# Optimization experiments

Hardware: AMD Instinct MI355X
Metric: run time of the kernel (lower is better)

The kernel has to match this reference:

```python
import jax, jax.numpy as jnp
import numpy as np

N = 50000   # nodes
E = 800000  # edges (before self-loops)
IN, H1, H2, OUT = 128, 256, 256, 64


def _gcn_layer(x, src, dst, norm_src, norm_dst, W, b, act):
    # DGL GraphConv, norm='both': D_in^{-1/2} * A^T * (D_out^{-1/2} * x) @ W + b
    x = x * norm_src                                   # [N, d_in]
    m = jax.ops.segment_sum(x[src], dst, num_segments=N)  # gather + scatter-add
    h = (m * norm_dst) @ W + b                         # [N, d_out]
    return act(h) if act is not None else h


def setup_inputs() -> dict:
    key = jax.random.key(0)
    ks = jax.random.split(key, 9)
    feats = jax.random.normal(ks[0], (N, IN), dtype=jnp.float32)
    src = jax.random.randint(ks[1], (E,), 0, N, dtype=jnp.int32)
    dst = jax.random.randint(ks[2], (E,), 0, N, dtype=jnp.int32)
    # avoid pre-existing self-loops (forward removes then re-adds exactly one per node)
    dst = jnp.where(src == dst, (dst + 1) % N, dst)
    def glorot(k, fi, fo):
        lim = float(np.sqrt(6.0 / (fi + fo)))
        return jax.random.uniform(k, (fi, fo), jnp.float32, -lim, lim)
    return {
        "feats": feats,
        "W1": glorot(ks[3], IN, H1), "b1": jnp.zeros((H1,), jnp.float32),
        "W2": glorot(ks[4], H1, H2), "b2": jnp.zeros((H2,), jnp.float32),
        "W3": glorot(ks[5], H2, OUT), "b3": jnp.zeros((OUT,), jnp.float32),
        "src": src, "dst": dst,
    }


def reference(feats, W1, b1, W2, b2, W3, b3, src, dst):
    # add self-loops
    loops = jnp.arange(N, dtype=src.dtype)
    s = jnp.concatenate([src, loops])
    d = jnp.concatenate([dst, loops])
    ones = jnp.ones(s.shape[0], jnp.float32)
    out_deg = jax.ops.segment_sum(ones, s, num_segments=N)
    in_deg = jax.ops.segment_sum(ones, d, num_segments=N)
    norm_src = (out_deg ** -0.5)[:, None]
    norm_dst = (in_deg ** -0.5)[:, None]
    relu = jax.nn.relu
    h = _gcn_layer(feats, s, d, norm_src, norm_dst, W1, b1, relu)
    # dropout p=0.0 (eval) is identity
    h = _gcn_layer(h, s, d, norm_src, norm_dst, W2, b2, relu)
    h = _gcn_layer(h, s, d, norm_src, norm_dst, W3, b3, None)
    return h
```

## Files before the change

### kernel.cpp

```cpp
#include <hip/hip_runtime.h>
#include <hip/hip_fp16.h>
#include <stdint.h>

#define NODES 50000
#define F_IN 128
#define F_H1 256
#define F_H2 256
#define F_OUT 64
#define SLICES 64
#define NPACK (NODES / 2)
#define QPACK (NPACK / 4)

using f32x4    = __attribute__((ext_vector_type(4))) float;
using f16x8    = __attribute__((ext_vector_type(8))) _Float16;
using ushort8v = __attribute__((ext_vector_type(8))) unsigned short;

__global__ __launch_bounds__(512) void k_hist2(
    const int* __restrict__ src, const int* __restrict__ dst,
    unsigned* __restrict__ p_out, unsigned* __restrict__ p_in, int e) {
  __shared__ unsigned bo[QPACK];
  __shared__ unsigned bi[QPACK];
  const int s = blockIdx.x >> 2;
  const int r = blockIdx.x & 3;
  const int nlo = r * (NODES / 4);
  const int nhi = nlo + NODES / 4;
  const int plo = r * QPACK;
  const int per = (e + SLICES - 1) / SLICES;
  const int beg = s * per;
  const int end = min(e, beg + per);

  for (int j = threadIdx.x; j < QPACK; j += 512) { bo[j] = 0; bi[j] = 0; }
  __syncthreads();
  for (int i = beg + (int)threadIdx.x; i < end; i += 512) {
    int a = src[i];
    if (a >= nlo && a < nhi)
      atomicAdd(&bo[(a >> 1) - plo], 1u << ((a & 1) << 4));
    int d = dst[i];
    if (d >= nlo && d < nhi)
      atomicAdd(&bi[(d >> 1) - plo], 1u << ((d & 1) << 4));
  }
  __syncthreads();
  for (int j = threadIdx.x; j < QPACK; j += 512) {
    p_out[(size_t)s * NPACK + plo + j] = bo[j];
    p_in[(size_t)s * NPACK + plo + j] = bi[j];
  }
}

__global__ __launch_bounds__(256) void k_degnorm(
    const unsigned* __restrict__ p_out, const unsigned* __restrict__ p_in,
    unsigned* __restrict__ base_in, int* __restrict__ deg_in,
    float* __restrict__ ns, float* __restrict__ nd) {
  int p = blockIdx.x * 256 + threadIdx.x;
  if (p >= NPACK) return;
  unsigned so = 0, si = 0;
#pragma unroll 4
  for (int s = 0; s < SLICES; ++s) {
    so += p_out[(size_t)s * NPACK + p];
    unsigned vi = p_in[(size_t)s * NPACK + p];
    base_in[(size_t)s * NPACK + p] = si;
    si += vi;
  }
  int o0 = (int)(so & 0xFFFFu) + 1, o1 = (int)(so >> 16) + 1;
  int i0 = (int)(si & 0xFFFFu) + 1, i1 = (int)(si >> 16) + 1;
  int n0 = p * 2, n1 = n0 + 1;
  deg_in[n0] = i0; deg_in[n1] = i1;
  ns[n0] = rsqrtf((float)o0); ns[n1] = rsqrtf((float)o1);
  nd[n0] = rsqrtf((float)i0); nd[n1] = rsqrtf((float)i1);
}

__global__ __launch_bounds__(256) void k_scan1(const int* __restrict__ deg_in,
                                               int* __restrict__ psum, int n) {
  int i = blockIdx.x * 256 + threadIdx.x;
  int v = (i < n) ? deg_in[i] - 1 : 0;
#pragma unroll
  for (int o = 1; o < 64; o <<= 1) v += __shfl_xor(v, o);
  __shared__ int ws[4];
  if ((threadIdx.x & 63) == 0) ws[threadIdx.x >> 6] = v;
  __syncthreads();
  if (threadIdx.x == 0) psum[blockIdx.x] = ws[0] + ws[1] + ws[2] + ws[3];
}

__global__ __launch_bounds__(256) void k_scan2(int* __restrict__ psum, int nb) {
  __shared__ int s[256];
  int t = threadIdx.x;
  int v = (t < nb) ? psum[t] : 0;
  s[t] = v;
  __syncthreads();
  for (int o = 1; o < 256; o <<= 1) {
    int u = (t >= o) ? s[t - o] : 0;
    __syncthreads();
    s[t] += u;
    __syncthreads();
  }
  if (t < nb) psum[t] = s[t] - v;
}

__global__ __launch_bounds__(256) void k_scan3(const int* __restrict__ deg_in,
                                               const int* __restrict__ psum,
                                               int* __restrict__ row_ptr, int n) {
  int i = blockIdx.x * 256 + threadIdx.x;
  int lane = threadIdx.x & 63;
  int w = threadIdx.x >> 6;
  int v = (i < n) ? deg_in[i] - 1 : 0;
  int x = v;
#pragma unroll
  for (int o = 1; o < 64; o <<= 1) {
    int u = __shfl_up(x, o);
    if (lane >= o) x += u;
  }
  __shared__ int wsum[4];
  if (lane == 63) wsum[w] = x;
  __syncthreads();
  int woff = 0;
#pragma unroll
  for (int j = 0; j < 4; ++j)
    if (j < w) woff += wsum[j];
  int excl = x - v + woff + psum[blockIdx.x];
  if (i < n) row_ptr[i] = excl;
  if (i == n - 1) row_ptr[n] = excl + v;
}

__global__ __launch_bounds__(512) void k_scatter4(
    const int* __restrict__ src, const int* __restrict__ dst,
    const int* __restrict__ row_ptr, const unsigned* __restrict__ base_in,
    int* __restrict__ csr_src, int e) {
  __shared__ unsigned cur[QPACK];
  const int s = blockIdx.x >> 2;
  const int r = blockIdx.x & 3;
  const int nlo = r * (NODES / 4);
  const int nhi = nlo + NODES / 4;
  const int plo = r * QPACK;
  const int per = (e + SLICES - 1) / SLICES;
  const int beg = s * per;
  const int end = min(e, beg + per);
  for (int j = threadIdx.x; j < QPACK; j += 512)
    cur[j] = base_in[(size_t)s * NPACK + plo + j];
  __syncthreads();
  for (int i = beg + (int)threadIdx.x; i < end; i += 512) {
    int d = dst[i];
    if (d >= nlo && d < nhi) {
      int sh = (d & 1) << 4;
      unsigned old = atomicAdd(&cur[(d >> 1) - plo], 1u << sh);
      int local = (int)((old >> sh) & 0xFFFFu);
      csr_src[row_ptr[d] + local] = src[i];
    }
  }
}

__global__ void k_prescale_h(const float* __restrict__ X, const float* __restrict__ ns,
                             __half* __restrict__ Y, int total4) {
  int i = blockIdx.x * blockDim.x + threadIdx.x;
  if (i < total4) {
    int row = i >> 5;
    float s = ns[row];
    float4 v = reinterpret_cast<const float4*>(X)[i];
    __half2 h0 = __floats2half2_rn(v.x * s, v.y * s);
    __half2 h1 = __floats2half2_rn(v.z * s, v.w * s);
    union { struct { __half2 a, b; } h; uint2 u; } o;
    o.h.a = h0; o.h.b = h1;
    reinterpret_cast<uint2*>(Y)[i] = o.u;
  }
}

__global__ void k_wprep_h(const float* __restrict__ W, __half* __restrict__ Wt,
                          int K, int NOUT) {
  int i = blockIdx.x * blockDim.x + threadIdx.x;
  if (i < K * NOUT) {
    int k = i / NOUT, n = i % NOUT;
    Wt[(size_t)n * K + k] = __float2half_rn(W[i]);
  }
}

struct u32x8s { uint4 a, b; };
template <int HPL> struct raw_t_sel;
template <> struct raw_t_sel<2> { using type = unsigned int; };
template <> struct raw_t_sel<4> { using type = uint2; };
template <> struct raw_t_sel<8> { using type = uint4; };
template <> struct raw_t_sel<16> { using type = u32x8s; };

template <int HPL>
__device__ __forceinline__ typename raw_t_sel<HPL>::type graw(const __half* p) {
  if constexpr (HPL == 16) {
    u32x8s r;
    r.a = *reinterpret_cast<const uint4*>(p);
    r.b = *reinterpret_cast<const uint4*>(p + 8);
    return r;
  } else {
    return *reinterpret_cast<const typename raw_t_sel<HPL>::type*>(p);
  }
}
__device__ __forceinline__ void acc_u32(float* acc, unsigned u) {
  union { unsigned u; __half2 h; } a; a.u = u;
  float2 f = __half22float2(a.h);
  acc[0] += f.x; acc[1] += f.y;
}
template <int HPL>
__device__ __forceinline__ void raw_acc(float* acc, typename raw_t_sel<HPL>::type r) {
  if constexpr (HPL == 16) {
    acc_u32(acc + 0, r.a.x);  acc_u32(acc + 2, r.a.y);
    acc_u32(acc + 4, r.a.z);  acc_u32(acc + 6, r.a.w);
    acc_u32(acc + 8, r.b.x);  acc_u32(acc + 10, r.b.y);
    acc_u32(acc + 12, r.b.z); acc_u32(acc + 14, r.b.w);
  } else if constexpr (HPL == 8) {
    acc_u32(acc + 0, r.x); acc_u32(acc + 2, r.y);
    acc_u32(acc + 4, r.z); acc_u32(acc + 6, r.w);
  } else if constexpr (HPL == 4) {
    acc_u32(acc + 0, r.x); acc_u32(acc + 2, r.y);
  } else {
    acc_u32(acc, r);
  }
}

template <int D, int EPI, bool BIAS, bool OHALF>
__global__ __launch_bounds__(256) void k_spmm_h(
    const __half* __restrict__ X, const int* __restrict__ row_ptr,
    const int* __restrict__ csr_src, const float* __restrict__ nd,
    const float* __restrict__ bias, void* __restrict__ Y, int n) {
  constexpr int LPN = 64 / EPI;
  constexpr int HPL = D / LPN;
  static_assert(HPL >= 2 && HPL <= 16, "bad HPL");
  const int v = (blockIdx.x * blockDim.x + threadIdx.x) >> 6;
  const int lane = threadIdx.x & 63;
  if (v >= n) return;
  const int sub = lane / LPN;
  const int fl = lane % LPN;
  const int off = fl * HPL;
  const __half* __restrict__ Xo = X + off;

  float acc[HPL] = {};
  if (sub == 0) raw_acc<HPL>(acc, graw<HPL>(Xo + (size_t)v * D));

  const int beg = row_ptr[v];
  const int end = row_ptr[v + 1];
#pragma unroll 2
  for (int e = beg + sub; e < end; e += EPI) {
    int u = csr_src[e];
    raw_acc<HPL>(acc, graw<HPL>(Xo + (size_t)u * D));
  }

#pragma unroll
  for (int o = LPN; o < 64; o <<= 1)
#pragma unroll
    for (int i = 0; i < HPL; ++i) acc[i] += __shfl_xor(acc[i], o);

  if (sub != 0) return;
  const float sc = nd[v];
  float o[HPL];
#pragma unroll
  for (int i = 0; i < HPL; ++i) {
    o[i] = sc * acc[i];
    if (BIAS) o[i] += bias[off + i];
  }

  if constexpr (OHALF) {
    __half* yp = reinterpret_cast<__half*>(Y) + (size_t)v * D + off;
    if constexpr (HPL == 16) {
      union { struct { __half2 a, b, c, d; } h; uint4 u; } p0, p1;
      p0.h.a = __floats2half2_rn(o[0], o[1]);
      p0.h.b = __floats2half2_rn(o[2], o[3]);
      p0.h.c = __floats2half2_rn(o[4], o[5]);
      p0.h.d = __floats2half2_rn(o[6], o[7]);
      p1.h.a = __floats2half2_rn(o[8], o[9]);
      p1.h.b = __floats2half2_rn(o[10], o[11]);
      p1.h.c = __floats2half2_rn(o[12], o[13]);
      p1.h.d = __floats2half2_rn(o[14], o[15]);
      *reinterpret_cast<uint4*>(yp) = p0.u;
      *reinterpret_cast<uint4*>(yp + 8) = p1.u;
    } else if constexpr (HPL == 8) {
      union { struct { __half2 a, b, c, d; } h; uint4 u; } pk;
      pk.h.a = __floats2half2_rn(o[0], o[1]);
      pk.h.b = __floats2half2_rn(o[2], o[3]);
      pk.h.c = __floats2half2_rn(o[4], o[5]);
      pk.h.d = __floats2half2_rn(o[6], o[7]);
      *reinterpret_cast<uint4*>(yp) = pk.u;
    } else if constexpr (HPL == 4) {
      union { struct { __half2 a, b; } h; uint2 u; } pk;
      pk.h.a = __floats2half2_rn(o[0], o[1]);
      pk.h.b = __floats2half2_rn(o[2], o[3]);
      *reinterpret_cast<uint2*>(yp) = pk.u;
    } else {
      *reinterpret_cast<__half2*>(yp) = __floats2half2_rn(o[0], o[1]);
    }
  } else {
    float* yp = reinterpret_cast<float*>(Y) + (size_t)v * D + off;
    if constexpr (HPL == 8) {
      *reinterpret_cast<float4*>(yp) = make_float4(o[0], o[1], o[2], o[3]);
      *reinterpret_cast<float4*>(yp + 4) = make_float4(o[4], o[5], o[6], o[7]);
    } else if constexpr (HPL == 4) {
      *reinterpret_cast<float4*>(yp) = make_float4(o[0], o[1], o[2], o[3]);
    } else {
      *reinterpret_cast<float2*>(yp) = make_float2(o[0], o[1]);
    }
  }
}

template <int K, int NOUT, int BM, int WM, int WN, int MF, int NF,
          bool RELU, bool BIAS, bool NSOUT, bool OHALF>
__global__ __launch_bounds__(256) void k_gemm_h(
    const __half* __restrict__ A, const __half* __restrict__ Wt,
    const float* __restrict__ bias, const float* __restrict__ ns,
    void* __restrict__ C, int M) {
  constexpr int BN = WN * NF * 16;
  static_assert(BM == WM * MF * 16, "BM mismatch");
  static_assert(BN == NOUT, "BN must equal NOUT");
  constexpr int LDP = 40;

  __shared__ __half As[BM][LDP];
  __shared__ __half Ws[BN][LDP];

  const int tid = threadIdx.x;
  const int bm = blockIdx.x * BM;
  const int lane = tid & 63;
  const int wave = tid >> 6;
  const int wmi = wave / WN;
  const int wni = wave % WN;
  const int rl = lane & 15;
  const int kg = lane >> 4;
  const int kb = kg * 8;

  f32x4 acc[MF][NF];
#pragma unroll
  for (int m = 0; m < MF; ++m)
#pragma unroll
    for (int n = 0; n < NF; ++n) acc[m][n] = (f32x4){0.f, 0.f, 0.f, 0.f};

  for (int kk = 0; kk < K; kk += 32) {
#pragma unroll
    for (int s0 = 0; s0 < BM * 4; s0 += 256) {
      int s = s0 + tid;
      int r = s >> 2, c8 = (s & 3) << 3;
      int grow = bm + r;
      ushort8v v = (ushort8v){0, 0, 0, 0, 0, 0, 0, 0};
      if (grow < M)
        v = *reinterpret_cast<const ushort8v*>(A + (size_t)grow * K + kk + c8);
      *reinterpret_cast<ushort8v*>(&As[r][c8]) = v;
    }
#pragma unroll
    for (int s0 = 0; s0 < BN * 4; s0 += 256) {
      int s = s0 + tid;
      int nn = s >> 2, k8 = (s & 3) << 3;
      *reinterpret_cast<ushort8v*>(&Ws[nn][k8]) =
          *reinterpret_cast<const ushort8v*>(Wt + (size_t)nn * K + kk + k8);
    }
    __syncthreads();

    f16x8 af[MF], bf[NF];
#pragma unroll
    for (int m = 0; m < MF; ++m) {
      const int r = wmi * MF * 16 + m * 16 + rl;
      af[m] = *reinterpret_cast<const f16x8*>(&As[r][kb]);
    }
#pragma unroll
    for (int n = 0; n < NF; ++n) {
      const int c = wni * NF * 16 + n * 16 + rl;
      bf[n] = *reinterpret_cast<const f16x8*>(&Ws[c][kb]);
    }
#pragma unroll
    for (int m = 0; m < MF; ++m)
#pragma unroll
      for (int n = 0; n < NF; ++n)
        acc[m][n] = __builtin_amdgcn_mfma_f32_16x16x32_f16(af[m], bf[n], acc[m][n], 0, 0, 0);
    __syncthreads();
  }

#pragma unroll
  for (int m = 0; m < MF; ++m) {
#pragma unroll
    for (int n = 0; n < NF; ++n) {
      const int col = wni * NF * 16 + n * 16 + rl;
      const float bb = BIAS ? bias[col] : 0.f;
      const int rowbase = bm + wmi * MF * 16 + m * 16 + kg * 4;
#pragma unroll
      for (int i = 0; i < 4; ++i) {
        int grow = rowbase + i;
        if (grow < M) {
          float val = acc[m][n][i] + bb;
          if (RELU) val = fmaxf(val, 0.f);
          if (NSOUT) val *= ns[grow];
          if constexpr (OHALF)
            reinterpret_cast<__half*>(C)[(size_t)grow * NOUT + col] = __float2half_rn(val);
          else
            reinterpret_cast<float*>(C)[(size_t)grow * NOUT + col] = val;
        }
      }
    }
  }
}

extern "C" void kernel_launch(void* const* d_in, const int* in_sizes, int n_in,
                              void* d_out, int out_size, void* d_ws, size_t ws_size,
                              hipStream_t stream) {
  const float* feats = (const float*)d_in[0];
  const float* W1 = (const float*)d_in[1];
  const float* b1 = (const float*)d_in[2];
  const float* W2 = (const float*)d_in[3];
  const float* b2 = (const float*)d_in[4];
  const float* W3 = (const float*)d_in[5];
  const float* b3 = (const float*)d_in[6];
  const int* src = (const int*)d_in[7];
  const int* dst = (const int*)d_in[8];
  float* out = (float*)d_out;
  const int N = NODES;
  const int E = in_sizes[7];
  const int NB = (N + 255) / 256;

  char* ws = (char*)d_ws;
  size_t off = 0;
  auto alloc = [&](size_t bytes) -> void* {
    void* p = ws + off;
    off += (bytes + 255) & ~(size_t)255;
    return p;
  };
  __half* w0h = (__half*)alloc((size_t)N * 256 * sizeof(__half));
  __half* w1r = (__half*)alloc((size_t)N * 256 * sizeof(__half));
  __half* w2r = (__half*)alloc((size_t)N * 256 * sizeof(__half));
  int* deg_in = (int*)alloc((size_t)N * sizeof(int));
  float* ns = (float*)alloc((size_t)N * sizeof(float));
  float* nd = (float*)alloc((size_t)N * sizeof(float));
  int* row_ptr = (int*)alloc((size_t)(N + 1) * sizeof(int));
  int* csr_src = (int*)alloc((size_t)E * sizeof(int));
  int* psum = (int*)alloc((size_t)NB * sizeof(int));
  unsigned* p_out = (unsigned*)alloc((size_t)SLICES * NPACK * sizeof(unsigned));
  unsigned* p_in = (unsigned*)alloc((size_t)SLICES * NPACK * sizeof(unsigned));
  unsigned* base_in = (unsigned*)alloc((size_t)SLICES * NPACK * sizeof(unsigned));
  __half* wt1 = (__half*)alloc((size_t)F_IN * F_H1 * sizeof(__half));
  __half* wt2 = (__half*)alloc((size_t)F_H1 * F_H2 * sizeof(__half));
  __half* wt3 = (__half*)alloc((size_t)F_H2 * F_OUT * sizeof(__half));
  (void)ws_size; (void)n_in; (void)out_size;

  hipLaunchKernelGGL(k_wprep_h, dim3((F_IN * F_H1 + 255) / 256), dim3(256), 0, stream,
                     W1, wt1, F_IN, F_H1);
  hipLaunchKernelGGL(k_wprep_h, dim3((F_H1 * F_H2 + 255) / 256), dim3(256), 0, stream,
                     W2, wt2, F_H1, F_H2);
  hipLaunchKernelGGL(k_wprep_h, dim3((F_H2 * F_OUT + 255) / 256), dim3(256), 0, stream,
                     W3, wt3, F_H2, F_OUT);

  hipLaunchKernelGGL(k_hist2, dim3(SLICES * 4), dim3(512), 0, stream,
                     src, dst, p_out, p_in, E);
  hipLaunchKernelGGL(k_degnorm, dim3((NPACK + 255) / 256), dim3(256), 0, stream,
                     p_out, p_in, base_in, deg_in, ns, nd);
  hipLaunchKernelGGL(k_scan1, dim3(NB), dim3(256), 0, stream, deg_in, psum, N);
  hipLaunchKernelGGL(k_scan2, dim3(1), dim3(256), 0, stream, psum, NB);
  hipLaunchKernelGGL(k_scan3, dim3(NB), dim3(256), 0, stream, deg_in, psum, row_ptr, N);
  hipLaunchKernelGGL(k_scatter4, dim3(SLICES * 4), dim3(512), 0, stream,
                     src, dst, row_ptr, base_in, csr_src, E);

  hipLaunchKernelGGL(k_prescale_h, dim3((N * 32 + 255) / 256), dim3(256), 0, stream,
                     feats, ns, w2r, N * 32);

  auto grid_w = [](int waves) { return dim3((waves + 3) / 4); };

  hipLaunchKernelGGL((k_spmm_h<128, 8, false, true>), grid_w(N), dim3(256), 0, stream,
                     w2r, row_ptr, csr_src, nd, nullptr, w1r, N);
  hipLaunchKernelGGL((k_gemm_h<128, 256, 64, 1, 4, 4, 4, true, true, true, true>),
                     dim3((N + 63) / 64), dim3(256), 0, stream,
                     w1r, wt1, b1, ns, w2r, N);

  hipLaunchKernelGGL((k_spmm_h<256, 4, false, true>), grid_w(N), dim3(256), 0, stream,
                     w2r, row_ptr, csr_src, nd, nullptr, w0h, N);
  hipLaunchKernelGGL((k_gemm_h<256, 256, 64, 1, 4, 4, 4, true, true, true, true>),
                     dim3((N + 63) / 64), dim3(256), 0, stream,
                     w0h, wt2, b2, ns, w1r, N);

  hipLaunchKernelGGL((k_gemm_h<256, 64, 128, 4, 1, 2, 4, false, false, false, true>),
                     dim3((N + 127) / 128), dim3(256), 0, stream,
                     w1r, wt3, nullptr, nullptr, w2r, N);
  hipLaunchKernelGGL((k_spmm_h<64, 8, true, false>), grid_w(N), dim3(256), 0, stream,
                     w2r, row_ptr, csr_src, nd, b3, out, N);
}
```

Baseline: 261.8 us.

## Fuse SpMM aggregation with GEMM for layers one and two; merge weight prep

Adds a fused kernel that gathers and aggregates neighbour rows for a 64-node tile straight into shared memory, then runs an MFMA GEMM with bias, ReLU and source-norm scaling. This removes the intermediate aggregated-feature buffer round trip through global memory and one launch per layer. The three weight-transpose launches are also merged into one. In exchange, each wave now processes 16 nodes serially in the gather phase, and the GEMM stage reloads weight tiles with a sync every K step and writes scalar half outputs, which may reduce gather parallelism and store efficiency.

```diff
diff --git a/kernel.cpp b/kernel.cpp
--- a/kernel.cpp
+++ b/kernel.cpp
@@ -162,12 +162,21 @@
   }
 }
 
-__global__ void k_wprep_h(const float* __restrict__ W, __half* __restrict__ Wt,
-                          int K, int NOUT) {
-  int i = blockIdx.x * blockDim.x + threadIdx.x;
-  if (i < K * NOUT) {
-    int k = i / NOUT, n = i % NOUT;
-    Wt[(size_t)n * K + k] = __float2half_rn(W[i]);
+__global__ void k_wprep_all(const float* __restrict__ W1, const float* __restrict__ W2,
+                            const float* __restrict__ W3, __half* __restrict__ wt1,
+                            __half* __restrict__ wt2, __half* __restrict__ wt3) {
+  int i = blockIdx.x * 256 + threadIdx.x;
+  if (i < F_IN * F_H1) {
+    int k = i >> 8, n = i & 255;
+    wt1[(size_t)n * F_IN + k] = __float2half_rn(W1[i]);
+  } else if (i < F_IN * F_H1 + F_H1 * F_H2) {
+    int j = i - F_IN * F_H1;
+    int k = j >> 8, n = j & 255;
+    wt2[(size_t)n * F_H1 + k] = __float2half_rn(W2[j]);
+  } else if (i < F_IN * F_H1 + F_H1 * F_H2 + F_H2 * F_OUT) {
+    int j = i - F_IN * F_H1 - F_H1 * F_H2;
+    int k = j >> 6, n = j & 63;
+    wt3[(size_t)n * F_H2 + k] = __float2half_rn(W3[j]);
   }
 }
 
@@ -208,6 +217,118 @@
     acc_u32(acc + 0, r.x); acc_u32(acc + 2, r.y);
   } else {
     acc_u32(acc, r);
+  }
+}
+
+template <int K>
+__global__ __launch_bounds__(256) void k_fused(
+    const __half* __restrict__ X, const int* __restrict__ row_ptr,
+    const int* __restrict__ csr_src, const float* __restrict__ nd,
+    const __half* __restrict__ Wt, const float* __restrict__ bias,
+    const float* __restrict__ ns, __half* __restrict__ C, int M) {
+  constexpr int BN = 256;
+  constexpr int LPN = K / 16;
+  constexpr int EPI = 64 / LPN;
+  constexpr int LDPA = K + 8;
+  constexpr int LDPB = 40;
+
+  __shared__ __half As[64][LDPA];
+  __shared__ __half Ws[BN][LDPB];
+
+  const int tid = threadIdx.x;
+  const int bm = blockIdx.x * 64;
+  const int lane = tid & 63;
+  const int wave = tid >> 6;
+  const int sub = lane / LPN;
+  const int fl = lane % LPN;
+  const int off = fl * 16;
+
+  for (int t = 0; t < 16; ++t) {
+    const int r = wave * 16 + t;
+    const int v = bm + r;
+    float acc[16] = {};
+    if (v < M) {
+      const __half* __restrict__ Xo = X + off;
+      if (sub == 0) raw_acc<16>(acc, graw<16>(Xo + (size_t)v * K));
+      const int beg = row_ptr[v];
+      const int end = row_ptr[v + 1];
+#pragma unroll 2
+      for (int e = beg + sub; e < end; e += EPI)
+        raw_acc<16>(acc, graw<16>(Xo + (size_t)csr_src[e] * K));
+    }
+#pragma unroll
+    for (int o = LPN; o < 64; o <<= 1)
+#pragma unroll
+      for (int i = 0; i < 16; ++i) acc[i] += __shfl_xor(acc[i], o);
+    if (sub == 0) {
+      const float sc = (v < M) ? nd[v] : 0.f;
+      union { struct { __half2 a, b, c, d; } h; uint4 u; } p0, p1;
+      p0.h.a = __floats2half2_rn(sc * acc[0], sc * acc[1]);
+      p0.h.b = __floats2half2_rn(sc * acc[2], sc * acc[3]);
+      p0.h.c = __floats2half2_rn(sc * acc[4], sc * acc[5]);
+      p0.h.d = __floats2half2_rn(sc * acc[6], sc * acc[7]);
+      p1.h.a = __floats2half2_rn(sc * acc[8], sc * acc[9]);
+      p1.h.b = __floats2half2_rn(sc * acc[10], sc * acc[11]);
+      p1.h.c = __floats2half2_rn(sc * acc[12], sc * acc[13]);
+      p1.h.d = __floats2half2_rn(sc * acc[14], sc * acc[15]);
+      *reinterpret_cast<uint4*>(&As[r][off]) = p0.u;
+      *reinterpret_cast<uint4*>(&As[r][off + 8]) = p1.u;
+    }
+  }
+  __syncthreads();
+
+  const int wni = wave;
+  const int rl = lane & 15;
+  const int kg = lane >> 4;
+  const int kb = kg * 8;
+
+  f32x4 acc2[4][4];
+#pragma unroll
+  for (int m = 0; m < 4; ++m)
+#pragma unroll
+    for (int n = 0; n < 4; ++n) acc2[m][n] = (f32x4){0.f, 0.f, 0.f, 0.f};
+
+  for (int kk = 0; kk < K; kk += 32) {
+#pragma unroll
+    for (int s0 = 0; s0 < BN * 4; s0 += 256) {
+      int s = s0 + tid;
+      int nn = s >> 2, k8 = (s & 3) << 3;
+      *reinterpret_cast<ushort8v*>(&Ws[nn][k8]) =
+          *reinterpret_cast<const ushort8v*>(Wt + (size_t)nn * K + kk + k8);
+    }
+    __syncthreads();
+
+    f16x8 af[4], bf[4];
+#pragma unroll
+    for (int m = 0; m < 4; ++m)
+      af[m] = *reinterpret_cast<const f16x8*>(&As[m * 16 + rl][kk + kb]);
+#pragma unroll
+    for (int n = 0; n < 4; ++n)
+      bf[n] = *reinterpret_cast<const f16x8*>(&Ws[wni * 64 + n * 16 + rl][kb]);
+#pragma unroll
+    for (int m = 0; m < 4; ++m)
+#pragma unroll
+      for (int n = 0; n < 4; ++n)
+        acc2[m][n] = __builtin_amdgcn_mfma_f32_16x16x32_f16(af[m], bf[n], acc2[m][n], 0, 0, 0);
+    __syncthreads();
+  }
+
+#pragma unroll
+  for (int m = 0; m < 4; ++m) {
+#pragma unroll
+    for (int n = 0; n < 4; ++n) {
+      const int col = wni * 64 + n * 16 + rl;
+      const float bb = bias[col];
+      const int rowbase = bm + m * 16 + kg * 4;
+#pragma unroll
+      for (int i = 0; i < 4; ++i) {
+        int grow = rowbase + i;
+        if (grow < M) {
+          float val = fmaxf(acc2[m][n][i] + bb, 0.f) * ns[grow];
+          C[(size_t)grow * BN + col] = __float2half_rn(val);
+        }
+      }
+    }
   }
 }
 
@@ -254,19 +375,7 @@
 
   if constexpr (OHALF) {
     __half* yp = reinterpret_cast<__half*>(Y) + (size_t)v * D + off;
-    if constexpr (HPL == 16) {
-      union { struct { __half2 a, b, c, d; } h; uint4 u; } p0, p1;
-      p0.h.a = __floats2half2_rn(o[0], o[1]);
-      p0.h.b = __floats2half2_rn(o[2], o[3]);
-      p0.h.c = __floats2half2_rn(o[4], o[5]);
-      p0.h.d = __floats2half2_rn(o[6], o[7]);
-      p1.h.a = __floats2half2_rn(o[8], o[9]);
-      p1.h.b = __floats2half2_rn(o[10], o[11]);
-      p1.h.c = __floats2half2_rn(o[12], o[13]);
-      p1.h.d = __floats2half2_rn(o[14], o[15]);
-      *reinterpret_cast<uint4*>(yp) = p0.u;
-      *reinterpret_cast<uint4*>(yp + 8) = p1.u;
-    } else if constexpr (HPL == 8) {
+    if constexpr (HPL == 8) {
       union { struct { __half2 a, b, c, d; } h; uint4 u; } pk;
       pk.h.a = __floats2half2_rn(o[0], o[1]);
       pk.h.b = __floats2half2_rn(o[2], o[3]);
@@ -428,12 +537,9 @@
   __half* wt3 = (__half*)alloc((size_t)F_H2 * F_OUT * sizeof(__half));
   (void)ws_size; (void)n_in; (void)out_size;
 
-  hipLaunchKernelGGL(k_wprep_h, dim3((F_IN * F_H1 + 255) / 256), dim3(256), 0, stream,
-                     W1, wt1, F_IN, F_H1);
-  hipLaunchKernelGGL(k_wprep_h, dim3((F_H1 * F_H2 + 255) / 256), dim3(256), 0, stream,
-                     W2, wt2, F_H1, F_H2);
-  hipLaunchKernelGGL(k_wprep_h, dim3((F_H2 * F_OUT + 255) / 256), dim3(256), 0, stream,
-                     W3, wt3, F_H2, F_OUT);
+  const int WPTOT = F_IN * F_H1 + F_H1 * F_H2 + F_H2 * F_OUT;
+  hipLaunchKernelGGL(k_wprep_all, dim3((WPTOT + 255) / 256), dim3(256), 0, stream,
+                     W1, W2, W3, wt1, wt2, wt3);
 
   hipLaunchKernelGGL(k_hist2, dim3(SLICES * 4), dim3(512), 0, stream,
                      src, dst, p_out, p_in, E);
@@ -448,23 +554,15 @@
   hipLaunchKernelGGL(k_prescale_h, dim3((N * 32 + 255) / 256), dim3(256), 0, stream,
                      feats, ns, w2r, N * 32);
 
-  auto grid_w = [](int waves) { return dim3((waves + 3) / 4); };
-
-  hipLaunchKernelGGL((k_spmm_h<128, 8, false, true>), grid_w(N), dim3(256), 0, stream,
-                     w2r, row_ptr, csr_src, nd, nullptr, w1r, N);
-  hipLaunchKernelGGL((k_gemm_h<128, 256, 64, 1, 4, 4, 4, true, true, true, true>),
-                     dim3((N + 63) / 64), dim3(256), 0, stream,
-                     w1r, wt1, b1, ns, w2r, N);
-
-  hipLaunchKernelGGL((k_spmm_h<256, 4, false, true>), grid_w(N), dim3(256), 0, stream,
-                     w2r, row_ptr, csr_src, nd, nullptr, w0h, N);
-  hipLaunchKernelGGL((k_gemm_h<256, 256, 64, 1, 4, 4, 4, true, true, true, true>),
-                     dim3((N + 63) / 64), dim3(256), 0, stream,
-                     w0h, wt2, b2, ns, w1r, N);
+  hipLaunchKernelGGL((k_fused<128>), dim3((N + 63) / 64), dim3(256), 0, stream,
+                     w2r, row_ptr, csr_src, nd, wt1, b1, ns, w1r, N);
+
+  hipLaunchKernelGGL((k_fused<256>), dim3((N + 63) / 64), dim3(256), 0, stream,
+                     w1r, row_ptr, csr_src, nd, wt2, b2, ns, w0h, N);
 
   hipLaunchKernelGGL((k_gemm_h<256, 64, 128, 4, 1, 2, 4, false, false, false, true>),
                      dim3((N + 127) / 128), dim3(256), 0, stream,
-                     w1r, wt3, nullptr, nullptr, w2r, N);
-  hipLaunchKernelGGL((k_spmm_h<64, 8, true, false>), grid_w(N), dim3(256), 0, stream,
+                     w0h, wt3, nullptr, nullptr, w2r, N);
+  hipLaunchKernelGGL((k_spmm_h<64, 8, true, false>), dim3((N + 3) / 4), dim3(256), 0, stream,
                      w2r, row_ptr, csr_src, nd, b3, out, N);
 }
```

Measured after the change: 352.2 us. +34.5%, slower.

## Fuse degree-norm and scan into one cooperative kernel; merge weight prep into prescale

Applied to the files above, without the earlier changes.

Replaces the degnorm plus three-kernel scan chain with a single cooperative kernel that computes norms, does block-local scans, takes a grid sync, then turns block sums into row pointers. The three weight transpose/convert launches are folded into the feature prescale kernel. The aim is fewer kernel launches and less launch/serialization overhead in the preprocessing stage. The price is a grid-wide barrier and a cooperative launch that needs all 196 blocks co-resident.

```diff
diff --git a/kernel.cpp b/kernel.cpp
--- a/kernel.cpp
+++ b/kernel.cpp
@@ -1,6 +1,9 @@
 #include <hip/hip_runtime.h>
 #include <hip/hip_fp16.h>
+#include <hip/hip_cooperative_groups.h>
 #include <stdint.h>
+
+namespace cg = cooperative_groups;
 
 #define NODES 50000
 #define F_IN 128
@@ -10,6 +13,7 @@
 #define SLICES 64
 #define NPACK (NODES / 2)
 #define QPACK (NPACK / 4)
+#define META_B 196
 
 using f32x4    = __attribute__((ext_vector_type(4))) float;
 using f16x8    = __attribute__((ext_vector_type(8))) _Float16;
@@ -46,78 +50,70 @@
   }
 }
 
-__global__ __launch_bounds__(256) void k_degnorm(
+__global__ __launch_bounds__(256) void k_csrmeta(
     const unsigned* __restrict__ p_out, const unsigned* __restrict__ p_in,
-    unsigned* __restrict__ base_in, int* __restrict__ deg_in,
-    float* __restrict__ ns, float* __restrict__ nd) {
-  int p = blockIdx.x * 256 + threadIdx.x;
-  if (p >= NPACK) return;
-  unsigned so = 0, si = 0;
+    unsigned* __restrict__ base_in, float* __restrict__ ns, float* __restrict__ nd,
+    int* __restrict__ psum, int* __restrict__ row_ptr) {
+  const int b = blockIdx.x;
+  const int t = threadIdx.x;
+  const int lane = t & 63;
+  const int w = t >> 6;
+  __shared__ int degm1[256];
+  __shared__ int wsum[4];
+  __shared__ int bsum[4];
+
+  int d0 = 0, d1 = 0;
+  if (t < 128) {
+    int p = b * 128 + t;
+    if (p < NPACK) {
+      unsigned so = 0, si = 0;
 #pragma unroll 4
-  for (int s = 0; s < SLICES; ++s) {
-    so += p_out[(size_t)s * NPACK + p];
-    unsigned vi = p_in[(size_t)s * NPACK + p];
-    base_in[(size_t)s * NPACK + p] = si;
-    si += vi;
-  }
-  int o0 = (int)(so & 0xFFFFu) + 1, o1 = (int)(so >> 16) + 1;
-  int i0 = (int)(si & 0xFFFFu) + 1, i1 = (int)(si >> 16) + 1;
-  int n0 = p * 2, n1 = n0 + 1;
-  deg_in[n0] = i0; deg_in[n1] = i1;
-  ns[n0] = rsqrtf((float)o0); ns[n1] = rsqrtf((float)o1);
-  nd[n0] = rsqrtf((float)i0); nd[n1] = rsqrtf((float)i1);
-}
-
-__global__ __launch_bounds__(256) void k_scan1(const int* __restrict__ deg_in,
-                                               int* __restrict__ psum, int n) {
-  int i = blockIdx.x * 256 + threadIdx.x;
-  int v = (i < n) ? deg_in[i] - 1 : 0;
-#pragma unroll
-  for (int o = 1; o < 64; o <<= 1) v += __shfl_xor(v, o);
-  __shared__ int ws[4];
-  if ((threadIdx.x & 63) == 0) ws[threadIdx.x >> 6] = v;
-  __syncthreads();
-  if (threadIdx.x == 0) psum[blockIdx.x] = ws[0] + ws[1] + ws[2] + ws[3];
-}
-
-__global__ __launch_bounds__(256) void k_scan2(int* __restrict__ psum, int nb) {
-  __shared__ int s[256];
-  int t = threadIdx.x;
-  int v = (t < nb) ? psum[t] : 0;
-  s[t] = v;
-  __syncthreads();
-  for (int o = 1; o < 256; o <<= 1) {
-    int u = (t >= o) ? s[t - o] : 0;
-    __syncthreads();
-    s[t] += u;
-    __syncthreads();
-  }
-  if (t < nb) psum[t] = s[t] - v;
-}
-
-__global__ __launch_bounds__(256) void k_scan3(const int* __restrict__ deg_in,
-                                               const int* __restrict__ psum,
-                                               int* __restrict__ row_ptr, int n) {
-  int i = blockIdx.x * 256 + threadIdx.x;
-  int lane = threadIdx.x & 63;
-  int w = threadIdx.x >> 6;
-  int v = (i < n) ? deg_in[i] - 1 : 0;
+      for (int s = 0; s < SLICES; ++s) {
+        so += p_out[(size_t)s * NPACK + p];
+        unsigned vi = p_in[(size_t)s * NPACK + p];
+        base_in[(size_t)s * NPACK + p] = si;
+        si += vi;
+      }
+      int o0 = (int)(so & 0xFFFFu) + 1, o1 = (int)(so >> 16) + 1;
+      int i0 = (int)(si & 0xFFFFu) + 1, i1 = (int)(si >> 16) + 1;
+      int n0 = p * 2, n1 = n0 + 1;
+      ns[n0] = rsqrtf((float)o0); ns[n1] = rsqrtf((float)o1);
+      nd[n0] = rsqrtf((float)i0); nd[n1] = rsqrtf((float)i1);
+      d0 = i0 - 1; d1 = i1 - 1;
+    }
+    degm1[2 * t] = d0;
+    degm1[2 * t + 1] = d1;
+  }
+  __syncthreads();
+
+  const int v = degm1[t];
   int x = v;
 #pragma unroll
   for (int o = 1; o < 64; o <<= 1) {
     int u = __shfl_up(x, o);
     if (lane >= o) x += u;
   }
-  __shared__ int wsum[4];
   if (lane == 63) wsum[w] = x;
   __syncthreads();
+  if (t == 0) psum[b] = wsum[0] + wsum[1] + wsum[2] + wsum[3];
+
+  cg::this_grid().sync();
+
+  int pv = (t < b) ? psum[t] : 0;
+#pragma unroll
+  for (int o = 1; o < 64; o <<= 1) pv += __shfl_xor(pv, o);
+  if (lane == 0) bsum[w] = pv;
+  __syncthreads();
+  const int prefix = bsum[0] + bsum[1] + bsum[2] + bsum[3];
+
   int woff = 0;
 #pragma unroll
   for (int j = 0; j < 4; ++j)
     if (j < w) woff += wsum[j];
-  int excl = x - v + woff + psum[blockIdx.x];
-  if (i < n) row_ptr[i] = excl;
-  if (i == n - 1) row_ptr[n] = excl + v;
+  const int excl = (x - v) + woff + prefix;
+  const int node = b * 256 + t;
+  if (node < NODES) row_ptr[node] = excl;
+  if (node == NODES - 1) row_ptr[NODES] = excl + v;
 }
 
 __global__ __launch_bounds__(512) void k_scatter4(
@@ -147,10 +143,14 @@
   }
 }
 
-__global__ void k_prescale_h(const float* __restrict__ X, const float* __restrict__ ns,
-                             __half* __restrict__ Y, int total4) {
-  int i = blockIdx.x * blockDim.x + threadIdx.x;
-  if (i < total4) {
+#define WPTOT (F_IN * F_H1 + F_H1 * F_H2 + F_H2 * F_OUT)
+__global__ void k_prewprep(const float* __restrict__ X, const float* __restrict__ ns,
+                           __half* __restrict__ Y,
+                           const float* __restrict__ W1, const float* __restrict__ W2,
+                           const float* __restrict__ W3, __half* __restrict__ wt1,
+                           __half* __restrict__ wt2, __half* __restrict__ wt3) {
+  int i = blockIdx.x * 256 + threadIdx.x;
+  if (i < NODES * 32) {
     int row = i >> 5;
     float s = ns[row];
     float4 v = reinterpret_cast<const float4*>(X)[i];
@@ -160,14 +160,19 @@
     o.h.a = h0; o.h.b = h1;
     reinterpret_cast<uint2*>(Y)[i] = o.u;
   }
-}
-
-__global__ void k_wprep_h(const float* __restrict__ W, __half* __restrict__ Wt,
-                          int K, int NOUT) {
-  int i = blockIdx.x * blockDim.x + threadIdx.x;
-  if (i < K * NOUT) {
-    int k = i / NOUT, n = i % NOUT;
-    Wt[(size_t)n * K + k] = __float2half_rn(W[i]);
+  if (i < WPTOT) {
+    if (i < F_IN * F_H1) {
+      int k = i >> 8, n = i & 255;
+      wt1[(size_t)n * F_IN + k] = __float2half_rn(W1[i]);
+    } else if (i < F_IN * F_H1 + F_H1 * F_H2) {
+      int j = i - F_IN * F_H1;
+      int k = j >> 8, n = j & 255;
+      wt2[(size_t)n * F_H1 + k] = __float2half_rn(W2[j]);
+    } else {
+      int j = i - F_IN * F_H1 - F_H1 * F_H2;
+      int k = j >> 6, n = j & 63;
+      wt3[(size_t)n * F_H2 + k] = __float2half_rn(W3[j]);
+    }
   }
 }
 
@@ -402,7 +407,6 @@
   float* out = (float*)d_out;
   const int N = NODES;
   const int E = in_sizes[7];
-  const int NB = (N + 255) / 256;
 
   char* ws = (char*)d_ws;
   size_t off = 0;
@@ -414,12 +418,11 @@
   __half* w0h = (__half*)alloc((size_t)N * 256 * sizeof(__half));
   __half* w1r = (__half*)alloc((size_t)N * 256 * sizeof(__half));
   __half* w2r = (__half*)alloc((size_t)N * 256 * sizeof(__half));
-  int* deg_in = (int*)alloc((size_t)N * sizeof(int));
   float* ns = (float*)alloc((size_t)N * sizeof(float));
   float* nd = (float*)alloc((size_t)N * sizeof(float));
   int* row_ptr = (int*)alloc((size_t)(N + 1) * sizeof(int));
   int* csr_src = (int*)alloc((size_t)E * sizeof(int));
-  int* psum = (int*)alloc((size_t)NB * sizeof(int));
+  int* psum = (int*)alloc((size_t)META_B * sizeof(int));
   unsigned* p_out = (unsigned*)alloc((size_t)SLICES * NPACK * sizeof(unsigned));
   unsigned* p_in = (unsigned*)alloc((size_t)SLICES * NPACK * sizeof(unsigned));
   unsigned* base_in = (unsigned*)alloc((size_t)SLICES * NPACK * sizeof(unsigned));
@@ -428,25 +431,20 @@
   __half* wt3 = (__half*)alloc((size_t)F_H2 * F_OUT * sizeof(__half));
   (void)ws_size; (void)n_in; (void)out_size;
 
-  hipLaunchKernelGGL(k_wprep_h, dim3((F_IN * F_H1 + 255) / 256), dim3(256), 0, stream,
-                     W1, wt1, F_IN, F_H1);
-  hipLaunchKernelGGL(k_wprep_h, dim3((F_H1 * F_H2 + 255) / 256), dim3(256), 0, stream,
-                     W2, wt2, F_H1, F_H2);
-  hipLaunchKernelGGL(k_wprep_h, dim3((F_H2 * F_OUT + 255) / 256), dim3(256), 0, stream,
-                     W3, wt3, F_H2, F_OUT);
-
   hipLaunchKernelGGL(k_hist2, dim3(SLICES * 4), dim3(512), 0, stream,
                      src, dst, p_out, p_in, E);
-  hipLaunchKernelGGL(k_degnorm, dim3((NPACK + 255) / 256), dim3(256), 0, stream,
-                     p_out, p_in, base_in, deg_in, ns, nd);
-  hipLaunchKernelGGL(k_scan1, dim3(NB), dim3(256), 0, stream, deg_in, psum, N);
-  hipLaunchKernelGGL(k_scan2, dim3(1), dim3(256), 0, stream, psum, NB);
-  hipLaunchKernelGGL(k_scan3, dim3(NB), dim3(256), 0, stream, deg_in, psum, row_ptr, N);
+
+  {
+    void* args[] = {(void*)&p_out, (void*)&p_in, (void*)&base_in, (void*)&ns,
+                    (void*)&nd, (void*)&psum, (void*)&row_ptr};
+    hipLaunchCooperativeKernel((void*)k_csrmeta, dim3(META_B), dim3(256), args, 0, stream);
+  }
+
   hipLaunchKernelGGL(k_scatter4, dim3(SLICES * 4), dim3(512), 0, stream,
                      src, dst, row_ptr, base_in, csr_src, E);
 
-  hipLaunchKernelGGL(k_prescale_h, dim3((N * 32 + 255) / 256), dim3(256), 0, stream,
-                     feats, ns, w2r, N * 32);
+  hipLaunchKernelGGL(k_prewprep, dim3((N * 32 + 255) / 256), dim3(256), 0, stream,
+                     feats, ns, w2r, W1, W2, W3, wt1, wt2, wt3);
 
   auto grid_w = [](int waves) { return dim3((waves + 3) / 4); };
 
@@ -465,6 +463,6 @@
   hipLaunchKernelGGL((k_gemm_h<256, 64, 128, 4, 1, 2, 4, false, false, false, true>),
                      dim3((N + 127) / 128), dim3(256), 0, stream,
                      w1r, wt3, nullptr, nullptr, w2r, N);
-  hipLaunchKernelGGL((k_spmm_h<64, 8, true, false>), grid_w(N), dim3(256), 0, stream,
+  hipLaunchKernelGGL((k_spmm_h<64, 8, true, false>), dim3((N + 3) / 4), dim3(256), 0, stream,
                      w2r, row_ptr, csr_src, nd, b3, out, N);
 }
```

Result: slower. 282.3 us (+7.8%).
